# Kernel tuning notes

Hardware: AMD Instinct MI355X
Metric: run time of the kernel (lower is better)

The kernel has to match this reference:

```python
import jax, jax.numpy as jnp
import numpy as np

ALPHA = 0.9

def setup_inputs() -> dict:
    key = jax.random.key(0)
    k1, k2 = jax.random.split(key)
    x = jax.random.normal(k1, (1024, 32, 1024), dtype=jnp.float32)
    state = jax.random.normal(k2, (32, 1024), dtype=jnp.float32)
    return {"x": x, "state": state}

def reference(x, state):
    # EMA recurrence: s_t = alpha * s_{t-1} + (1 - alpha) * x_t
    def step(s, xt):
        s = xt * (1.0 - ALPHA) + s * ALPHA
        return s, s
    final_state, out = jax.lax.scan(step, state, x)
    return out, final_state
```

## Files before the change

kernel.cpp:

```cpp
#include <hip/hip_runtime.h>


typedef float f32x4 __attribute__((ext_vector_type(4)));

constexpr int T = 1024;
constexpr int C = 32 * 1024;
constexpr int CV = C / 4;
constexpr int CHUNK = 64;
constexpr int NCHUNK = T / CHUNK;
constexpr float A64 = 1.1790184577738602e-3f;

__global__ __launch_bounds__(256)
void ExponentialDecay_23708219474744_locals(const f32x4* __restrict__ x4,
                                            f32x4* __restrict__ L) {
    const int cv = blockIdx.x * blockDim.x + threadIdx.x;
    const int c = blockIdx.y;
    const f32x4* __restrict__ xp = x4 + (size_t)c * CHUNK * CV + cv;

    const float a = 0.9f, oma = 0.1f;
    f32x4 s = {0.0f, 0.0f, 0.0f, 0.0f};
    #pragma unroll 8
    for (int t = 0; t < CHUNK; ++t) {
        f32x4 v = xp[(size_t)t * CV];
        s.x = fmaf(s.x, a, v.x * oma);
        s.y = fmaf(s.y, a, v.y * oma);
        s.z = fmaf(s.z, a, v.z * oma);
        s.w = fmaf(s.w, a, v.w * oma);
    }
    L[(size_t)c * CV + cv] = s;
}

__global__ __launch_bounds__(256)
void ExponentialDecay_23708219474744_kernel(const f32x4* __restrict__ x4,
                                            const f32x4* __restrict__ state4,
                                            const f32x4* __restrict__ L,
                                            f32x4* __restrict__ out4) {
    const int cv = blockIdx.x * blockDim.x + threadIdx.x;
    const int c = blockIdx.y;
    const float a = 0.9f, oma = 0.1f;

    f32x4 s = state4[cv];
    for (int j = 0; j < c; ++j) {
        f32x4 l = L[(size_t)j * CV + cv];
        s.x = fmaf(s.x, A64, l.x);
        s.y = fmaf(s.y, A64, l.y);
        s.z = fmaf(s.z, A64, l.z);
        s.w = fmaf(s.w, A64, l.w);
    }

    const f32x4* __restrict__ xp = x4 + (size_t)c * CHUNK * CV + cv;
    f32x4* __restrict__ op = out4 + (size_t)c * CHUNK * CV + cv;

    #pragma unroll 8
    for (int t = 0; t < CHUNK; ++t) {
        f32x4 v = xp[(size_t)t * CV];
        s.x = fmaf(s.x, a, v.x * oma);
        s.y = fmaf(s.y, a, v.y * oma);
        s.z = fmaf(s.z, a, v.z * oma);
        s.w = fmaf(s.w, a, v.w * oma);
        op[(size_t)t * CV] = s;
    }

    if (c == NCHUNK - 1) {
        out4[(size_t)T * CV + cv] = s;
    }
}

extern "C" void kernel_launch(void* const* d_in, const int* in_sizes, int n_in,
                              void* d_out, int out_size, void* d_ws, size_t ws_size,
                              hipStream_t stream) {
    const f32x4* x = (const f32x4*)d_in[0];
    const f32x4* state = (const f32x4*)d_in[1];
    f32x4* out = (f32x4*)d_out;
    f32x4* L = (f32x4*)d_ws;

    dim3 block(256);
    dim3 grid1(CV / 256, NCHUNK - 1);
    ExponentialDecay_23708219474744_locals<<<grid1, block, 0, stream>>>(x, L);

    dim3 grid2(CV / 256, NCHUNK);
    ExponentialDecay_23708219474744_kernel<<<grid2, block, 0, stream>>>(x, state, L, out);
}
```

Before: 255.8 us.

## Switch chunked EMA to three-phase scan with small chunks and separate carry scan

Chunk length drops from 64 to 8 time steps. A dedicated scan kernel now computes the per-chunk starting states sequentially into workspace, replacing the quadratic carry loop that each block previously ran over all earlier chunk summaries. Locals and output kernels use 1024-thread blocks, each thread handling 4 strided vectors. This raises parallelism and removes redundant carry work, but adds a third launch and extra workspace traffic (L and S arrays of 128 chunks). It also relies on the workspace being large enough for both arrays.

New measurement: 288.9 us. +12.9%, slower.

```diff
diff --git a/kernel.cpp b/kernel.cpp
--- a/kernel.cpp
+++ b/kernel.cpp
@@ -6,63 +6,90 @@
 constexpr int T = 1024;
 constexpr int C = 32 * 1024;
 constexpr int CV = C / 4;
-constexpr int CHUNK = 64;
+constexpr int CHUNK = 8;
 constexpr int NCHUNK = T / CHUNK;
-constexpr float A64 = 1.1790184577738602e-3f;
+constexpr int SPLIT = 2;
+constexpr int HALF = CV / SPLIT;
+constexpr int V = 4;
+constexpr float A8 = 0.43046721f;
 
-__global__ __launch_bounds__(256)
+__global__ __launch_bounds__(1024)
 void ExponentialDecay_23708219474744_locals(const f32x4* __restrict__ x4,
-                                            f32x4* __restrict__ L) {
-    const int cv = blockIdx.x * blockDim.x + threadIdx.x;
+                                            f32x4* __restrict__ L4) {
+    const int td = threadIdx.x;
     const int c = blockIdx.y;
-    const f32x4* __restrict__ xp = x4 + (size_t)c * CHUNK * CV + cv;
+    const int col0 = blockIdx.x * HALF + (td >> 6) * (64 * V) + (td & 63);
+    const f32x4* __restrict__ xp = x4 + (size_t)c * CHUNK * CV + col0;
 
-    const float a = 0.9f, oma = 0.1f;
-    f32x4 s = {0.0f, 0.0f, 0.0f, 0.0f};
-    #pragma unroll 8
+    f32x4 s[V] = {};
+    #pragma unroll
     for (int t = 0; t < CHUNK; ++t) {
-        f32x4 v = xp[(size_t)t * CV];
-        s.x = fmaf(s.x, a, v.x * oma);
-        s.y = fmaf(s.y, a, v.y * oma);
-        s.z = fmaf(s.z, a, v.z * oma);
-        s.w = fmaf(s.w, a, v.w * oma);
+        #pragma unroll
+        for (int j = 0; j < V; ++j) {
+            f32x4 v = xp[(size_t)t * CV + j * 64];
+            s[j].x = fmaf(s[j].x, 0.9f, v.x * 0.1f);
+            s[j].y = fmaf(s[j].y, 0.9f, v.y * 0.1f);
+            s[j].z = fmaf(s[j].z, 0.9f, v.z * 0.1f);
+            s[j].w = fmaf(s[j].w, 0.9f, v.w * 0.1f);
+        }
     }
-    L[(size_t)c * CV + cv] = s;
+    #pragma unroll
+    for (int j = 0; j < V; ++j)
+        L4[(size_t)c * CV + col0 + j * 64] = s[j];
 }
 
 __global__ __launch_bounds__(256)
+void ExponentialDecay_23708219474744_scan(const f32x4* __restrict__ state4,
+                                          const f32x4* __restrict__ L4,
+                                          f32x4* __restrict__ S4) {
+    const int col = blockIdx.x * 256 + threadIdx.x;
+    f32x4 s = state4[col];
+    #pragma unroll 8
+    for (int c = 0; c < NCHUNK; ++c) {
+        S4[(size_t)c * CV + col] = s;
+        if (c < NCHUNK - 1) {
+            f32x4 l = L4[(size_t)c * CV + col];
+            s.x = fmaf(s.x, A8, l.x);
+            s.y = fmaf(s.y, A8, l.y);
+            s.z = fmaf(s.z, A8, l.z);
+            s.w = fmaf(s.w, A8, l.w);
+        }
+    }
+}
+
+__global__ __launch_bounds__(1024)
 void ExponentialDecay_23708219474744_kernel(const f32x4* __restrict__ x4,
-                                            const f32x4* __restrict__ state4,
-                                            const f32x4* __restrict__ L,
+                                            const f32x4* __restrict__ S4,
                                             f32x4* __restrict__ out4) {
-    const int cv = blockIdx.x * blockDim.x + threadIdx.x;
+    const int td = threadIdx.x;
     const int c = blockIdx.y;
-    const float a = 0.9f, oma = 0.1f;
+    const int col0 = blockIdx.x * HALF + (td >> 6) * (64 * V) + (td & 63);
 
-    f32x4 s = state4[cv];
-    for (int j = 0; j < c; ++j) {
-        f32x4 l = L[(size_t)j * CV + cv];
-        s.x = fmaf(s.x, A64, l.x);
-        s.y = fmaf(s.y, A64, l.y);
-        s.z = fmaf(s.z, A64, l.z);
-        s.w = fmaf(s.w, A64, l.w);
-    }
+    f32x4 s[V];
+    #pragma unroll
+    for (int j = 0; j < V; ++j)
+        s[j] = S4[(size_t)c * CV + col0 + j * 64];
 
-    const f32x4* __restrict__ xp = x4 + (size_t)c * CHUNK * CV + cv;
-    f32x4* __restrict__ op = out4 + (size_t)c * CHUNK * CV + cv;
+    const f32x4* __restrict__ xp = x4 + (size_t)c * CHUNK * CV + col0;
+    f32x4* __restrict__ op = out4 + (size_t)c * CHUNK * CV + col0;
 
-    #pragma unroll 8
+    #pragma unroll
     for (int t = 0; t < CHUNK; ++t) {
-        f32x4 v = xp[(size_t)t * CV];
-        s.x = fmaf(s.x, a, v.x * oma);
-        s.y = fmaf(s.y, a, v.y * oma);
-        s.z = fmaf(s.z, a, v.z * oma);
-        s.w = fmaf(s.w, a, v.w * oma);
-        op[(size_t)t * CV] = s;
+        #pragma unroll
+        for (int j = 0; j < V; ++j) {
+            f32x4 v = xp[(size_t)t * CV + j * 64];
+            s[j].x = fmaf(s[j].x, 0.9f, v.x * 0.1f);
+            s[j].y = fmaf(s[j].y, 0.9f, v.y * 0.1f);
+            s[j].z = fmaf(s[j].z, 0.9f, v.z * 0.1f);
+            s[j].w = fmaf(s[j].w, 0.9f, v.w * 0.1f);
+            op[(size_t)t * CV + j * 64] = s[j];
+        }
     }
 
     if (c == NCHUNK - 1) {
-        out4[(size_t)T * CV + cv] = s;
+        #pragma unroll
+        for (int j = 0; j < V; ++j)
+            out4[(size_t)T * CV + col0 + j * 64] = s[j];
     }
 }
 
@@ -73,11 +100,14 @@
     const f32x4* state = (const f32x4*)d_in[1];
     f32x4* out = (f32x4*)d_out;
     f32x4* L = (f32x4*)d_ws;
+    f32x4* S = L + (size_t)(NCHUNK - 1) * CV;
 
-    dim3 block(256);
-    dim3 grid1(CV / 256, NCHUNK - 1);
-    ExponentialDecay_23708219474744_locals<<<grid1, block, 0, stream>>>(x, L);
+    dim3 blk(1024);
+    dim3 g1(SPLIT, NCHUNK - 1);
+    ExponentialDecay_23708219474744_locals<<<g1, blk, 0, stream>>>(x, L);
 
-    dim3 grid2(CV / 256, NCHUNK);
-    ExponentialDecay_23708219474744_kernel<<<grid2, block, 0, stream>>>(x, state, L, out);
+    ExponentialDecay_23708219474744_scan<<<dim3(CV / 256), dim3(256), 0, stream>>>(state, L, S);
+
+    dim3 g2(SPLIT, NCHUNK);
+    ExponentialDecay_23708219474744_kernel<<<g2, blk, 0, stream>>>(x, S, out);
 }
```
